# Kernel optimization log

Hardware: AMD Instinct MI355X
Metric: run time of the kernel (lower is better)

## Reference

```python
import jax, jax.numpy as jnp
import numpy as np

B, T, C, H = 4, 4096, 512, 64

def setup_inputs() -> dict:
    key = jax.random.key(0)
    kx, kk, kq, kv = jax.random.split(key, 4)
    return {
        "x": jax.random.normal(kx, (B, T, C), dtype=jnp.float32),
        "Wk": jax.random.normal(kk, (C, H), dtype=jnp.float32) * (C ** -0.5),
        "Wq": jax.random.normal(kq, (C, H), dtype=jnp.float32) * (C ** -0.5),
        "Wv": jax.random.normal(kv, (C, H), dtype=jnp.float32) * (C ** -0.5),
    }

def reference(x, Wk, Wq, Wv):
    # x: [B, T, C]; bias-free projections to head_size H
    k = x @ Wk  # [B, T, H]
    q = x @ Wq  # [B, T, H]
    v = x @ Wv  # [B, T, H]
    channels = x.shape[-1]
    # NOTE: original scales by channels**-0.5 (embedding dim), not head_size
    scale = jnp.asarray(channels, x.dtype) ** -0.5
    wei = jnp.einsum("bth,bsh->bts", q, k) * scale  # [B, T, T]
    t = x.shape[1]
    causal = jnp.tril(jnp.ones((t, t), dtype=bool))
    wei = jnp.where(causal, wei, -jnp.inf)
    wei = jax.nn.softmax(wei, axis=-1)
    out = jnp.einsum("bts,bsh->bth", wei, v)  # [B, T, H]
    return out
```

## Files before the change

### kernel.cpp

```cpp
#include <hip/hip_runtime.h>


typedef __attribute__((ext_vector_type(8))) __bf16 bf16x8;
typedef __attribute__((ext_vector_type(8))) unsigned short u16x8;
typedef __attribute__((ext_vector_type(4))) float f32x4;

#define B_ 4
#define T_ 4096
#define C_ 512
#define H_ 64
#define BT (B_ * T_)

#define QSCALE (0.04419417382415922f * 1.4426950408889634f)

__device__ __forceinline__ unsigned short f2bf(float f) {
    unsigned int u = __builtin_bit_cast(unsigned int, f);
    u += 0x7fffu + ((u >> 16) & 1u);
    return (unsigned short)(u >> 16);
}

__device__ __forceinline__ unsigned int pkbf(float hi, float lo) {
    return __builtin_amdgcn_perm(__builtin_bit_cast(unsigned int, hi),
                                 __builtin_bit_cast(unsigned int, lo), 0x07060302u);
}

__device__ __forceinline__ float bf2f_lo(unsigned int u) {
    return __builtin_bit_cast(float, u << 16);
}
__device__ __forceinline__ float bf2f_hi(unsigned int u) {
    return __builtin_bit_cast(float, u & 0xffff0000u);
}

__device__ __forceinline__ f32x4 mfma16(bf16x8 a, bf16x8 b, f32x4 c) {
    return __builtin_amdgcn_mfma_f32_16x16x32_bf16(a, b, c, 0, 0, 0);
}

__global__ __launch_bounds__(256) void wt_kernel(const float* __restrict__ Wk,
                                                 const float* __restrict__ Wq,
                                                 const float* __restrict__ Wv,
                                                 unsigned short* __restrict__ Wtp) {
    int gid = blockIdx.x * 256 + threadIdx.x;
    int fidx = gid >> 9;
    int li = gid & 511;
    int lane = li >> 3, j = li & 7;
    int m3 = fidx / 64;
    int rem = fidx & 63;
    int nt = rem >> 4, kc = rem & 15;
    int h = nt * 16 + (lane & 15);
    int c = kc * 32 + (lane >> 4) * 8 + j;
    const float* W = (m3 == 0) ? Wk : ((m3 == 1) ? Wq : Wv);
    Wtp[gid] = f2bf(W[c * H_ + h]);
}

__global__ __launch_bounds__(256, 3) void proj_kernel(const float* __restrict__ x,
                                                      const unsigned short* __restrict__ Wtp,
                                                      unsigned short* __restrict__ Kf,
                                                      unsigned short* __restrict__ Qf,
                                                      unsigned short* __restrict__ Vf) {
    __shared__ __align__(16) char smem[2 * 64 * 52 * 4];
    float* Mg = (float*)smem;
    unsigned short* Ks_l = (unsigned short*)smem;
    unsigned short* Qs_l = Ks_l + 32 * 68;
    unsigned short* Vt_l = Qs_l + 32 * 68;

    const int tid = threadIdx.x;
    const int t0 = blockIdx.x * 32;
    const int wave = tid >> 6;
    const int ws = wave & 1;
    const int wh = wave >> 1;
    const int lane = tid & 63;
    const int lane15 = lane & 15;
    const int quad = lane >> 4;

    f32x4 acc[12];
#pragma unroll
    for (int i = 0; i < 12; ++i) acc[i] = (f32x4){0.f, 0.f, 0.f, 0.f};

    const float* xrow = x + (long)(t0 + ws * 16 + lane15) * C_;
    const unsigned short* wbase = Wtp + lane * 8;

    bf16x8 wf[12];
    float4 xa0[2], xa1[2];
    {
        const int kc0 = wh * 8;
        xa0[0] = *(const float4*)(xrow + kc0 * 32 + quad * 8);
        xa1[0] = *(const float4*)(xrow + kc0 * 32 + quad * 8 + 4);
        xa0[1] = *(const float4*)(xrow + (kc0 + 1) * 32 + quad * 8);
        xa1[1] = *(const float4*)(xrow + (kc0 + 1) * 32 + quad * 8 + 4);
#pragma unroll
        for (int i = 0; i < 12; ++i)
            wf[i] = *(const bf16x8*)(wbase + ((i * 16 + kc0) << 9));
    }

#pragma unroll
    for (int kk = 0; kk < 8; ++kk) {
        const int kc = wh * 8 + kk;
        const int cur = kk & 1;
        u16x8 t;
        t[0] = f2bf(xa0[cur].x); t[1] = f2bf(xa0[cur].y);
        t[2] = f2bf(xa0[cur].z); t[3] = f2bf(xa0[cur].w);
        t[4] = f2bf(xa1[cur].x); t[5] = f2bf(xa1[cur].y);
        t[6] = f2bf(xa1[cur].z); t[7] = f2bf(xa1[cur].w);
        bf16x8 a = __builtin_bit_cast(bf16x8, t);
        if (kk < 6) {
            xa0[cur] = *(const float4*)(xrow + (kc + 2) * 32 + quad * 8);
            xa1[cur] = *(const float4*)(xrow + (kc + 2) * 32 + quad * 8 + 4);
        }
        __builtin_amdgcn_s_setprio(1);
#pragma unroll
        for (int i = 0; i < 12; ++i) {
            acc[i] = mfma16(a, wf[i], acc[i]);
            if (kk < 7)
                wf[i] = *(const bf16x8*)(wbase + ((i * 16 + kc + 1) << 9));
        }
        __builtin_amdgcn_s_setprio(0);
    }

    if (wh == 1) {
        float* mg = Mg + (ws * 64 + lane) * 52;
#pragma unroll
        for (int i = 0; i < 12; ++i) *(f32x4*)(mg + i * 4) = acc[i];
    }
    __syncthreads();
    if (wh == 0) {
        const float* mg = Mg + (ws * 64 + lane) * 52;
#pragma unroll
        for (int i = 0; i < 12; ++i) acc[i] += *(const f32x4*)(mg + i * 4);
    }
    __syncthreads();

    if (wh == 0) {
#pragma unroll
        for (int nt = 0; nt < 4; ++nt) {
            int col = nt * 16 + lane15;
#pragma unroll
            for (int r = 0; r < 4; ++r) {
                int row_l = ws * 16 + quad * 4 + r;
                Ks_l[row_l * 68 + col] = f2bf(acc[0 * 4 + nt][r]);
                Qs_l[row_l * 68 + col] = f2bf(acc[1 * 4 + nt][r] * QSCALE);
                Vt_l[col * 34 + row_l] = f2bf(acc[2 * 4 + nt][r]);
            }
        }
    }
    __syncthreads();

    const int b = t0 >> 12;
    const int tloc = t0 & 4095;
    const int st = wave >> 1, kk = wave & 1;
    const long gs = (long)(b * 256 + (tloc >> 4) + st);
    bf16x8 kv = *(const bf16x8*)&Ks_l[(st * 16 + lane15) * 68 + kk * 32 + quad * 8];
    *(bf16x8*)&Kf[(gs * 2 + kk) * 512 + lane * 8] = kv;
    bf16x8 qv = *(const bf16x8*)&Qs_l[(st * 16 + lane15) * 68 + kk * 32 + quad * 8];
    *(bf16x8*)&Qf[(gs * 2 + kk) * 512 + lane * 8] = qv;
    const int hf = wave;
    const int vkk = (tloc >> 5) & 1;
    bf16x8 vv = *(const bf16x8*)&Vt_l[(hf * 16 + lane15) * 34 + quad * 8];
    const long sb = (long)(b * 64 + (tloc >> 6));
    *(bf16x8*)&Vf[(sb * 8 + hf * 2 + vkk) * 512 + lane * 8] = vv;
}

#define PSP 72

__global__ __launch_bounds__(256, 3) void attn_kernel(const unsigned short* __restrict__ Qf,
                                                      const unsigned short* __restrict__ Kf,
                                                      const unsigned short* __restrict__ Vf,
                                                      unsigned short* __restrict__ Opb,
                                                      float* __restrict__ lp,
                                                      float* __restrict__ out) {
    __shared__ __align__(16) unsigned short Ps[8 * 16 * PSP];

    const int tid = threadIdx.x;
    const int wave = tid >> 6;
    const int lane = tid & 63;
    const int lane15 = lane & 15;
    const int quad = lane >> 4;
    const int b = blockIdx.y;

    const int z = 287 - blockIdx.x;
    int g = (int)((__builtin_sqrtf((float)z + 1.0f) - 1.0f) * 0.5f);
    while (4 * (g + 1) * (g + 2) <= z) ++g;
    while (4 * g * (g + 1) > z) --g;
    const int idx = z - 4 * g * (g + 1);
    const int qt = g * 8 + idx / (g + 1);
    const int chunk = idx % (g + 1);
    const int ntt = min(8, qt + 1 - chunk * 8);
    const int t0k = chunk * 8;

    const long gs_q = (long)(b * 256 + qt * 4 + wave);
    const unsigned short* qb = Qf + gs_q * 1024 + lane * 8;
    const bf16x8 qf0 = *(const bf16x8*)qb;
    const bf16x8 qf1 = *(const bf16x8*)(qb + 512);

    f32x4 o_acc[4];
    f32x4 l_vec = (f32x4){0.f, 0.f, 0.f, 0.f};
#pragma unroll
    for (int hf = 0; hf < 4; ++hf) o_acc[hf] = (f32x4){0.f, 0.f, 0.f, 0.f};

    bf16x8 kf[8], vf[8];
    {
        const unsigned short* kb = Kf + (long)(b * 256 + t0k * 4) * 1024 + lane * 8;
        const unsigned short* vb = Vf + (long)(b * 64 + t0k) * 4096 + lane * 8;
#pragma unroll
        for (int ct = 0; ct < 4; ++ct) {
            kf[ct * 2 + 0] = *(const bf16x8*)(kb + ct * 1024);
            kf[ct * 2 + 1] = *(const bf16x8*)(kb + ct * 1024 + 512);
        }
#pragma unroll
        for (int f = 0; f < 8; ++f) vf[f] = *(const bf16x8*)(vb + f * 512);
    }

#pragma unroll 2
    for (int t = 0; t < ntt; ++t) {
        const int kc = t0k + t;
        const bool more = (t + 1 < ntt);
        const unsigned short* kbn = Kf + (long)(b * 256 + (kc + 1) * 4) * 1024 + lane * 8;
        const unsigned short* vbn = Vf + (long)(b * 64 + kc + 1) * 4096 + lane * 8;
        unsigned short* pw = Ps + ((wave << 1) | (t & 1)) * 16 * PSP;

        f32x4 st[4];
        __builtin_amdgcn_s_setprio(1);
#pragma unroll
        for (int ct = 0; ct < 4; ++ct) {
            f32x4 zz = (f32x4){0.f, 0.f, 0.f, 0.f};
            zz = mfma16(kf[ct * 2 + 0], qf0, zz);
            zz = mfma16(kf[ct * 2 + 1], qf1, zz);
            st[ct] = zz;
        }
        __builtin_amdgcn_s_setprio(0);

        if (more) {
#pragma unroll
            for (int ct = 0; ct < 4; ++ct) {
                kf[ct * 2 + 0] = *(const bf16x8*)(kbn + ct * 1024);
                kf[ct * 2 + 1] = *(const bf16x8*)(kbn + ct * 1024 + 512);
            }
        }

        if (kc == qt) {
            const int qg = wave * 16 + lane15;
#pragma unroll
            for (int ct = 0; ct < 4; ++ct) {
                const int sb = ct * 16 + quad * 4;
#pragma unroll
                for (int r = 0; r < 4; ++r)
                    if (sb + r > qg) st[ct][r] = -3.0e38f;
            }
        }

#pragma unroll
        for (int ct = 0; ct < 4; ++ct) {
#pragma unroll
            for (int r = 0; r < 4; ++r)
                st[ct][r] = __builtin_amdgcn_exp2f(st[ct][r]);
            l_vec += st[ct];
        }

#pragma unroll
        for (int ct = 0; ct < 4; ++ct) {
            unsigned int w0 = pkbf(st[ct][1], st[ct][0]);
            unsigned int w1 = pkbf(st[ct][3], st[ct][2]);
            *(uint2*)&pw[lane15 * PSP + ct * 16 + quad * 4] = make_uint2(w0, w1);
        }

        bf16x8 pa0 = *(const bf16x8*)&pw[lane15 * PSP + quad * 8];
        bf16x8 pa1 = *(const bf16x8*)&pw[lane15 * PSP + 32 + quad * 8];
        __builtin_amdgcn_s_setprio(1);
#pragma unroll
        for (int hf = 0; hf < 4; ++hf) {
            o_acc[hf] = mfma16(pa0, vf[hf * 2 + 0], o_acc[hf]);
            o_acc[hf] = mfma16(pa1, vf[hf * 2 + 1], o_acc[hf]);
        }
        __builtin_amdgcn_s_setprio(0);

        if (more) {
#pragma unroll
            for (int f = 0; f < 8; ++f) vf[f] = *(const bf16x8*)(vbn + f * 512);
        }
    }

    float l_acc = (l_vec[0] + l_vec[1]) + (l_vec[2] + l_vec[3]);
    l_acc += __shfl_xor(l_acc, 16);
    l_acc += __shfl_xor(l_acc, 32);

    if ((qt >> 3) == 0) {
        float linv[4];
#pragma unroll
        for (int r = 0; r < 4; ++r) linv[r] = 1.0f / __shfl(l_acc, quad * 4 + r);
        float* o = out + ((long)b * T_ + qt * 64 + wave * 16) * H_;
#pragma unroll
        for (int hf = 0; hf < 4; ++hf)
#pragma unroll
            for (int r = 0; r < 4; ++r)
                o[(quad * 4 + r) * H_ + hf * 16 + lane15] = o_acc[hf][r] * linv[r];
    } else {
        const long pbase = ((long)(b * 64 + qt) * 8 + chunk) * 64;
        if (quad == 0) lp[pbase + wave * 16 + lane15] = l_acc;
        unsigned short* op = Opb + (pbase + wave * 16) * 64;
#pragma unroll
        for (int hf = 0; hf < 4; ++hf)
#pragma unroll
            for (int r = 0; r < 4; ++r)
                op[(quad * 4 + r) * 64 + hf * 16 + lane15] = f2bf(o_acc[hf][r]);
    }
}

__global__ __launch_bounds__(256) void merge_kernel(const unsigned short* __restrict__ Opb,
                                                    const float* __restrict__ lp,
                                                    float* __restrict__ out) {
    const int qt = 8 + (blockIdx.x >> 1);
    const int rh = (blockIdx.x & 1) << 5;
    const int b = blockIdx.y;
    const int nc = 1 + (qt >> 3);
    const int tid = threadIdx.x;
    const int row = rh + (tid >> 3);
    const int seg = (tid & 7) << 3;

    const long base = (long)(b * 64 + qt) * 8;
    float l = 0.f;
    f32x4 a0 = (f32x4){0.f, 0.f, 0.f, 0.f};
    f32x4 a1 = (f32x4){0.f, 0.f, 0.f, 0.f};

#pragma unroll 2
    for (int c = 0; c < nc; ++c) {
        l += lp[(base + c) * 64 + row];
        const unsigned short* op = Opb + ((base + c) * 64 + row) * 64 + seg;
        uint4 d = *(const uint4*)op;
        a0[0] += bf2f_lo(d.x); a0[1] += bf2f_hi(d.x);
        a0[2] += bf2f_lo(d.y); a0[3] += bf2f_hi(d.y);
        a1[0] += bf2f_lo(d.z); a1[1] += bf2f_hi(d.z);
        a1[2] += bf2f_lo(d.w); a1[3] += bf2f_hi(d.w);
    }
    const float inv = 1.0f / l;
    float* o = out + ((long)b * T_ + qt * 64 + row) * H_ + seg;
    *(f32x4*)o = a0 * inv;
    *(f32x4*)(o + 4) = a1 * inv;
}

extern "C" void kernel_launch(void* const* d_in, const int* in_sizes, int n_in,
                              void* d_out, int out_size, void* d_ws, size_t ws_size,
                              hipStream_t stream) {
    const float* x  = (const float*)d_in[0];
    const float* Wk = (const float*)d_in[1];
    const float* Wq = (const float*)d_in[2];
    const float* Wv = (const float*)d_in[3];
    float* out = (float*)d_out;

    char* ws = (char*)d_ws;
    unsigned short* Kf  = (unsigned short*)(ws);
    unsigned short* Qf  = (unsigned short*)(ws + (2u << 20));
    unsigned short* Vf  = (unsigned short*)(ws + (4u << 20));
    unsigned short* Wtp = (unsigned short*)(ws + (6u << 20));
    unsigned short* Opb = (unsigned short*)(ws + (8u << 20));
    float* lp = (float*)(ws + (26u << 20));

    wt_kernel<<<384, 256, 0, stream>>>(Wk, Wq, Wv, Wtp);
    proj_kernel<<<BT / 32, 256, 0, stream>>>(x, Wtp, Kf, Qf, Vf);
    attn_kernel<<<dim3(288, B_), 256, 0, stream>>>(Qf, Kf, Vf, Opb, lp, out);
    merge_kernel<<<dim3(112, B_), 256, 0, stream>>>(Opb, lp, out);
}
```

Measured before the change: 115.5 us.

## Process two query tiles per attention block to reuse K/V fragments

Each attention block now handles 128 query rows, as two 64-row tiles, instead of 64. Every K/V fragment loaded from global memory feeds both tiles' QK and PV MFMAs, roughly halving K/V load traffic per query. The block-to-work mapping is rebuilt for 144 blocks per batch, with causal masking generalised to absolute key/query positions. In exchange, the grid holds half as many blocks, register and LDS use per block rise, and the first tile does wasted masked work on the diagonal tile belonging to the second.

```diff
diff --git a/kernel.cpp b/kernel.cpp
--- a/kernel.cpp
+++ b/kernel.cpp
@@ -167,7 +167,7 @@
                                                       unsigned short* __restrict__ Opb,
                                                       float* __restrict__ lp,
                                                       float* __restrict__ out) {
-    __shared__ __align__(16) unsigned short Ps[8 * 16 * PSP];
+    __shared__ __align__(16) unsigned short Ps[16 * 16 * PSP];
 
     const int tid = threadIdx.x;
     const int wave = tid >> 6;
@@ -176,25 +176,33 @@
     const int quad = lane >> 4;
     const int b = blockIdx.y;
 
-    const int z = 287 - blockIdx.x;
-    int g = (int)((__builtin_sqrtf((float)z + 1.0f) - 1.0f) * 0.5f);
-    while (4 * (g + 1) * (g + 2) <= z) ++g;
-    while (4 * g * (g + 1) > z) --g;
-    const int idx = z - 4 * g * (g + 1);
-    const int qt = g * 8 + idx / (g + 1);
+    const int z = 143 - blockIdx.x;
+    int g = (int)((__builtin_sqrtf(2.0f * (float)z + 1.0f) - 1.0f) * 0.5f);
+    while (2 * (g + 1) * (g + 2) <= z) ++g;
+    while (2 * g * (g + 1) > z) --g;
+    const int idx = z - 2 * g * (g + 1);
+    const int qmt = g * 4 + idx / (g + 1);
     const int chunk = idx % (g + 1);
-    const int ntt = min(8, qt + 1 - chunk * 8);
+    const int ntt = min(8, 2 * qmt + 2 - chunk * 8);
     const int t0k = chunk * 8;
-
-    const long gs_q = (long)(b * 256 + qt * 4 + wave);
-    const unsigned short* qb = Qf + gs_q * 1024 + lane * 8;
-    const bf16x8 qf0 = *(const bf16x8*)qb;
-    const bf16x8 qf1 = *(const bf16x8*)(qb + 512);
-
-    f32x4 o_acc[4];
-    f32x4 l_vec = (f32x4){0.f, 0.f, 0.f, 0.f};
-#pragma unroll
-    for (int hf = 0; hf < 4; ++hf) o_acc[hf] = (f32x4){0.f, 0.f, 0.f, 0.f};
+    const int dt0 = 2 * qmt, dt1 = 2 * qmt + 1;
+    const int qg0 = qmt * 128 + wave * 16 + lane15;
+
+    const long gq = (long)(b * 256 + qmt * 8 + wave);
+    const unsigned short* qb = Qf + gq * 1024 + lane * 8;
+    const bf16x8 qf00 = *(const bf16x8*)qb;
+    const bf16x8 qf01 = *(const bf16x8*)(qb + 512);
+    const bf16x8 qf10 = *(const bf16x8*)(qb + 4096);
+    const bf16x8 qf11 = *(const bf16x8*)(qb + 4096 + 512);
+
+    f32x4 o0[4], o1[4];
+    f32x4 lv0 = (f32x4){0.f, 0.f, 0.f, 0.f};
+    f32x4 lv1 = (f32x4){0.f, 0.f, 0.f, 0.f};
+#pragma unroll
+    for (int hf = 0; hf < 4; ++hf) {
+        o0[hf] = (f32x4){0.f, 0.f, 0.f, 0.f};
+        o1[hf] = (f32x4){0.f, 0.f, 0.f, 0.f};
+    }
 
     bf16x8 kf[8], vf[8];
     {
@@ -208,6 +216,8 @@
 #pragma unroll
         for (int f = 0; f < 8; ++f) vf[f] = *(const bf16x8*)(vb + f * 512);
     }
+
+    unsigned short* pwb = Ps + wave * 4 * 16 * PSP;
 
 #pragma unroll 2
     for (int t = 0; t < ntt; ++t) {
@@ -215,16 +225,52 @@
         const bool more = (t + 1 < ntt);
         const unsigned short* kbn = Kf + (long)(b * 256 + (kc + 1) * 4) * 1024 + lane * 8;
         const unsigned short* vbn = Vf + (long)(b * 64 + kc + 1) * 4096 + lane * 8;
-        unsigned short* pw = Ps + ((wave << 1) | (t & 1)) * 16 * PSP;
+        unsigned short* pw0 = pwb + (t & 1) * (2 * 16 * PSP);
+        unsigned short* pw1 = pw0 + 16 * PSP;
+        const int sbt = kc * 64;
 
         f32x4 st[4];
         __builtin_amdgcn_s_setprio(1);
 #pragma unroll
         for (int ct = 0; ct < 4; ++ct) {
             f32x4 zz = (f32x4){0.f, 0.f, 0.f, 0.f};
-            zz = mfma16(kf[ct * 2 + 0], qf0, zz);
-            zz = mfma16(kf[ct * 2 + 1], qf1, zz);
+            zz = mfma16(kf[ct * 2 + 0], qf00, zz);
+            zz = mfma16(kf[ct * 2 + 1], qf01, zz);
             st[ct] = zz;
+        }
+        __builtin_amdgcn_s_setprio(0);
+
+        if (kc >= dt0) {
+#pragma unroll
+            for (int ct = 0; ct < 4; ++ct) {
+                const int sb = sbt + ct * 16 + quad * 4;
+#pragma unroll
+                for (int r = 0; r < 4; ++r)
+                    if (sb + r > qg0) st[ct][r] = -3.0e38f;
+            }
+        }
+#pragma unroll
+        for (int ct = 0; ct < 4; ++ct) {
+#pragma unroll
+            for (int r = 0; r < 4; ++r)
+                st[ct][r] = __builtin_amdgcn_exp2f(st[ct][r]);
+            lv0 += st[ct];
+        }
+#pragma unroll
+        for (int ct = 0; ct < 4; ++ct) {
+            unsigned int w0 = pkbf(st[ct][1], st[ct][0]);
+            unsigned int w1 = pkbf(st[ct][3], st[ct][2]);
+            *(uint2*)&pw0[lane15 * PSP + ct * 16 + quad * 4] = make_uint2(w0, w1);
+        }
+
+        f32x4 su[4];
+        __builtin_amdgcn_s_setprio(1);
+#pragma unroll
+        for (int ct = 0; ct < 4; ++ct) {
+            f32x4 zz = (f32x4){0.f, 0.f, 0.f, 0.f};
+            zz = mfma16(kf[ct * 2 + 0], qf10, zz);
+            zz = mfma16(kf[ct * 2 + 1], qf11, zz);
+            su[ct] = zz;
         }
         __builtin_amdgcn_s_setprio(0);
 
@@ -236,39 +282,44 @@
             }
         }
 
-        if (kc == qt) {
-            const int qg = wave * 16 + lane15;
+        if (kc >= dt1) {
+            const int qg1 = qg0 + 64;
 #pragma unroll
             for (int ct = 0; ct < 4; ++ct) {
-                const int sb = ct * 16 + quad * 4;
+                const int sb = sbt + ct * 16 + quad * 4;
 #pragma unroll
                 for (int r = 0; r < 4; ++r)
-                    if (sb + r > qg) st[ct][r] = -3.0e38f;
+                    if (sb + r > qg1) su[ct][r] = -3.0e38f;
             }
         }
-
-#pragma unroll
-        for (int ct = 0; ct < 4; ++ct) {
-#pragma unroll
-            for (int r = 0; r < 4; ++r)
-                st[ct][r] = __builtin_amdgcn_exp2f(st[ct][r]);
-            l_vec += st[ct];
-        }
-
-#pragma unroll
-        for (int ct = 0; ct < 4; ++ct) {
-            unsigned int w0 = pkbf(st[ct][1], st[ct][0]);
-            unsigned int w1 = pkbf(st[ct][3], st[ct][2]);
-            *(uint2*)&pw[lane15 * PSP + ct * 16 + quad * 4] = make_uint2(w0, w1);
-        }
-
-        bf16x8 pa0 = *(const bf16x8*)&pw[lane15 * PSP + quad * 8];
-        bf16x8 pa1 = *(const bf16x8*)&pw[lane15 * PSP + 32 + quad * 8];
+#pragma unroll
+        for (int ct = 0; ct < 4; ++ct) {
+#pragma unroll
+            for (int r = 0; r < 4; ++r)
+                su[ct][r] = __builtin_amdgcn_exp2f(su[ct][r]);
+            lv1 += su[ct];
+        }
+#pragma unroll
+        for (int ct = 0; ct < 4; ++ct) {
+            unsigned int w0 = pkbf(su[ct][1], su[ct][0]);
+            unsigned int w1 = pkbf(su[ct][3], su[ct][2]);
+            *(uint2*)&pw1[lane15 * PSP + ct * 16 + quad * 4] = make_uint2(w0, w1);
+        }
+
+        bf16x8 pa00 = *(const bf16x8*)&pw0[lane15 * PSP + quad * 8];
+        bf16x8 pa01 = *(const bf16x8*)&pw0[lane15 * PSP + 32 + quad * 8];
+        bf16x8 pa10 = *(const bf16x8*)&pw1[lane15 * PSP + quad * 8];
+        bf16x8 pa11 = *(const bf16x8*)&pw1[lane15 * PSP + 32 + quad * 8];
         __builtin_amdgcn_s_setprio(1);
 #pragma unroll
         for (int hf = 0; hf < 4; ++hf) {
-            o_acc[hf] = mfma16(pa0, vf[hf * 2 + 0], o_acc[hf]);
-            o_acc[hf] = mfma16(pa1, vf[hf * 2 + 1], o_acc[hf]);
+            o0[hf] = mfma16(pa00, vf[hf * 2 + 0], o0[hf]);
+            o0[hf] = mfma16(pa01, vf[hf * 2 + 1], o0[hf]);
+        }
+#pragma unroll
+        for (int hf = 0; hf < 4; ++hf) {
+            o1[hf] = mfma16(pa10, vf[hf * 2 + 0], o1[hf]);
+            o1[hf] = mfma16(pa11, vf[hf * 2 + 1], o1[hf]);
         }
         __builtin_amdgcn_s_setprio(0);
 
@@ -278,29 +329,49 @@
         }
     }
 
-    float l_acc = (l_vec[0] + l_vec[1]) + (l_vec[2] + l_vec[3]);
-    l_acc += __shfl_xor(l_acc, 16);
-    l_acc += __shfl_xor(l_acc, 32);
-
-    if ((qt >> 3) == 0) {
-        float linv[4];
-#pragma unroll
-        for (int r = 0; r < 4; ++r) linv[r] = 1.0f / __shfl(l_acc, quad * 4 + r);
-        float* o = out + ((long)b * T_ + qt * 64 + wave * 16) * H_;
+    float l0 = (lv0[0] + lv0[1]) + (lv0[2] + lv0[3]);
+    l0 += __shfl_xor(l0, 16);
+    l0 += __shfl_xor(l0, 32);
+    float l1 = (lv1[0] + lv1[1]) + (lv1[2] + lv1[3]);
+    l1 += __shfl_xor(l1, 16);
+    l1 += __shfl_xor(l1, 32);
+
+    if (qmt < 4) {
+        float linv0[4], linv1[4];
+#pragma unroll
+        for (int r = 0; r < 4; ++r) {
+            linv0[r] = 1.0f / __shfl(l0, quad * 4 + r);
+            linv1[r] = 1.0f / __shfl(l1, quad * 4 + r);
+        }
+        float* o = out + ((long)b * T_ + qmt * 128 + wave * 16) * H_;
 #pragma unroll
         for (int hf = 0; hf < 4; ++hf)
 #pragma unroll
             for (int r = 0; r < 4; ++r)
-                o[(quad * 4 + r) * H_ + hf * 16 + lane15] = o_acc[hf][r] * linv[r];
+                o[(quad * 4 + r) * H_ + hf * 16 + lane15] = o0[hf][r] * linv0[r];
+        float* o2 = o + 64 * H_;
+#pragma unroll
+        for (int hf = 0; hf < 4; ++hf)
+#pragma unroll
+            for (int r = 0; r < 4; ++r)
+                o2[(quad * 4 + r) * H_ + hf * 16 + lane15] = o1[hf][r] * linv1[r];
     } else {
-        const long pbase = ((long)(b * 64 + qt) * 8 + chunk) * 64;
-        if (quad == 0) lp[pbase + wave * 16 + lane15] = l_acc;
-        unsigned short* op = Opb + (pbase + wave * 16) * 64;
+        const long pb0 = ((long)(b * 64 + dt0) * 8 + chunk) * 64;
+        if (quad == 0) lp[pb0 + wave * 16 + lane15] = l0;
+        unsigned short* op0 = Opb + (pb0 + wave * 16) * 64;
 #pragma unroll
         for (int hf = 0; hf < 4; ++hf)
 #pragma unroll
             for (int r = 0; r < 4; ++r)
-                op[(quad * 4 + r) * 64 + hf * 16 + lane15] = f2bf(o_acc[hf][r]);
+                op0[(quad * 4 + r) * 64 + hf * 16 + lane15] = f2bf(o0[hf][r]);
+        const long pb1 = ((long)(b * 64 + dt1) * 8 + chunk) * 64;
+        if (quad == 0) lp[pb1 + wave * 16 + lane15] = l1;
+        unsigned short* op1 = Opb + (pb1 + wave * 16) * 64;
+#pragma unroll
+        for (int hf = 0; hf < 4; ++hf)
+#pragma unroll
+            for (int r = 0; r < 4; ++r)
+                op1[(quad * 4 + r) * 64 + hf * 16 + lane15] = f2bf(o1[hf][r]);
     }
 }
 
@@ -355,6 +426,6 @@
 
     wt_kernel<<<384, 256, 0, stream>>>(Wk, Wq, Wv, Wtp);
     proj_kernel<<<BT / 32, 256, 0, stream>>>(x, Wtp, Kf, Qf, Vf);
-    attn_kernel<<<dim3(288, B_), 256, 0, stream>>>(Qf, Kf, Vf, Opb, lp, out);
+    attn_kernel<<<dim3(144, B_), 256, 0, stream>>>(Qf, Kf, Vf, Opb, lp, out);
     merge_kernel<<<dim3(112, B_), 256, 0, stream>>>(Opb, lp, out);
 }
```

Result: slower. 170.4 us (+47.5%).
